# Kernel tuning notes

Hardware: AMD Instinct MI355X
Metric: run time of the kernel (lower is better)

## Reference

```python
import jax, jax.numpy as jnp
import numpy as np
from jax import lax

B, H, W, CIN = 1, 100, 100, 1024
A = 9                      # len(anc_sizes)*len(anc_ratios)
C_BOT = 512
PRE, POST, IOU_THR = 6000, 300, 0.7   # eval path (training=False)


def setup_inputs() -> dict:
    key = jax.random.key(0)
    ks = jax.random.split(key, 9)
    std = 0.01  # RandomNormal(0, 0.01) as in the keras module
    feats = jax.random.normal(ks[0], (B, H, W, CIN), jnp.float32)
    centers = jax.random.uniform(ks[1], (B, H, W, A, 2), jnp.float32)
    wh = jax.random.uniform(ks[2], (B, H, W, A, 2), jnp.float32, minval=0.05, maxval=0.3)
    ancs = jnp.concatenate([centers, wh], axis=-1)          # ccwh, normalized
    ancs_valid = jnp.ones((B, H, W, A), jnp.float32)
    W_b = jax.random.normal(ks[3], (CIN, C_BOT), jnp.float32) * std
    b_b = jnp.zeros((C_BOT,), jnp.float32)
    W_cls = jax.random.normal(ks[4], (C_BOT, A), jnp.float32) * std
    b_cls = jnp.zeros((A,), jnp.float32)
    W_reg = jax.random.normal(ks[5], (C_BOT, A * 4), jnp.float32) * std
    b_reg = jnp.zeros((A * 4,), jnp.float32)
    return dict(feats=feats, ancs=ancs, ancs_valid=ancs_valid,
                W_b=W_b, b_b=b_b, W_cls=W_cls, b_cls=b_cls, W_reg=W_reg, b_reg=b_reg)


def _pairwise_iou(boxes):
    # boxes: [N,4] xyxy
    x1, y1, x2, y2 = boxes[:, 0], boxes[:, 1], boxes[:, 2], boxes[:, 3]
    area = (x2 - x1) * (y2 - y1)                              # [N]
    ix1 = jnp.maximum(x1[:, None], x1[None, :])
    iy1 = jnp.maximum(y1[:, None], y1[None, :])
    ix2 = jnp.minimum(x2[:, None], x2[None, :])
    iy2 = jnp.minimum(y2[:, None], y2[None, :])
    inter = jnp.maximum(ix2 - ix1, 0.0) * jnp.maximum(iy2 - iy1, 0.0)
    union = area[:, None] + area[None, :] - inter
    return inter / jnp.maximum(union, 1e-9)


def _nms_keep(boxes, valid):
    # greedy NMS over score-sorted boxes -> keep mask [N]
    iou = _pairwise_iou(boxes)
    n = boxes.shape[0]

    def step(keep_mask, i):
        suppressed = jnp.any(keep_mask & (iou[i] > IOU_THR))
        k = (~suppressed) & valid[i]
        return keep_mask.at[i].set(k), None

    keep, _ = lax.scan(step, jnp.zeros((n,), bool), jnp.arange(n))
    return keep


def _extract_proposals(cls_pred, reg_pred, ancs):
    grid_w, grid_h = cls_pred.shape[1], cls_pred.shape[2]
    scores = cls_pred.reshape(-1)           # [B*H*W*A]
    offs = reg_pred.reshape(-1, 4)
    anc = ancs.reshape(-1, 4)               # ccwh
    # apply_offsets: standard RPN decode
    xy = anc[:, :2] + offs[:, :2] * anc[:, 2:]
    wh = anc[:, 2:] * jnp.exp(offs[:, 2:])
    boxes = jnp.concatenate([xy - wh / 2, xy + wh / 2], axis=-1)   # ccwh -> xyxy
    boxes = jnp.clip(boxes, 0.0, 1.0)
    sizes = (boxes[:, 2:] - boxes[:, :2]) * jnp.array([grid_w, grid_h], jnp.float32)
    ok = jnp.all(sizes >= 1.0, axis=-1)
    # masked sort replaces boolean filtering (jit-safe); sigmoid scores are > 0,
    # so -1 marks filtered-out proposals
    masked = jnp.where(ok, scores, -1.0)
    top_scores, top_idx = lax.top_k(masked, PRE)     # descending
    top_boxes = boxes[top_idx]
    valid = top_scores > -0.5
    keep = _nms_keep(lax.stop_gradient(top_boxes), valid)
    # first POST kept boxes (in score order), zero-padded to fixed shape
    n = PRE
    prio = jnp.where(keep, jnp.arange(n), n + jnp.arange(n))
    order = jnp.argsort(prio)[:POST]
    out = jnp.where(keep[order][:, None], top_boxes[order], 0.0)
    return out


def reference(feats, ancs, ancs_valid, W_b, b_b, W_cls, b_cls, W_reg, b_reg):
    h = jax.nn.relu(jnp.einsum('bhwc,cd->bhwd', feats, W_b) + b_b)   # 1x1 conv
    cls_pred = jax.nn.sigmoid(jnp.einsum('bhwd,da->bhwa', h, W_cls) + b_cls)
    reg_pred = (jnp.einsum('bhwd,dk->bhwk', h, W_reg) + b_reg).reshape(B, H, W, A, 4)
    proposals = _extract_proposals(cls_pred, reg_pred, ancs)
    return cls_pred, reg_pred, proposals
```

## Files before the change

### kernel.cpp

```cpp
#include <hip/hip_runtime.h>
#include <math.h>

typedef unsigned int U32;
typedef unsigned long long U64;

#define NBOX   90000
#define NPIX   10000
#define KDIM   1024
#define CBOT   512
#define PRE_N  6000
#define POST_N 300
#define NWORD  94
#define MROWS  6016

#define OFF_H       0ULL
#define OFF_BOXES   20480000ULL
#define OFF_KEYS    21920000ULL
#define OFF_MASKT   22280000ULL
#define OFF_SEL     26804032ULL
#define OFF_SBOX    26852032ULL
#define OFF_VALIDW  26948032ULL
#define OFF_KEEPW   26948800ULL
#define OFF_HIST    26949568ULL
#define OFF_CNT     26950592ULL
#define OFF_TIE     26950848ULL
#define WS_NEED     26967232ULL


__global__ __launch_bounds__(256, 4) void k_gemm1(
    const float* __restrict__ A, const float* __restrict__ W,
    const float* __restrict__ bias, float* __restrict__ H,
    U32* __restrict__ hist, U32* __restrict__ cnt, U32* __restrict__ validw32)
{
  int t = threadIdx.x;
  if (blockIdx.x == 0) {
    hist[t] = 0;
    if (t < 64)  cnt[t] = (t == 1) ? (U32)PRE_N : 0u;
    if (t < 188) validw32[t] = 0;
  }
  int bid = blockIdx.x;
  int c = bid & 7;
  int s = bid >> 3;
  int x = s / 10;
  int yy = c * 10 + (s % 10);
  if (yy >= 79) return;
  __shared__ float As[16][132];
  __shared__ float Bs[16][68];
  int m0 = yy * 128, n0 = x * 64;
  int tm = t >> 4, tn = t & 15;
  int ar = t >> 1, ac = (t & 1) << 3;
  int bk = t >> 4, bc = (t & 15) << 2;
  float acc[8][4];
#pragma unroll
  for (int i = 0; i < 8; ++i)
#pragma unroll
    for (int j = 0; j < 4; ++j) acc[i][j] = 0.f;

  int arow = m0 + ar;
  float4 a0 = make_float4(0.f,0.f,0.f,0.f), a1 = a0;
  if (arow < NPIX) {
    a0 = *(const float4*)&A[(size_t)arow * KDIM + ac];
    a1 = *(const float4*)&A[(size_t)arow * KDIM + ac + 4];
  }
  float4 b0 = *(const float4*)&W[(size_t)bk * CBOT + n0 + bc];

  for (int k0 = 0; k0 < KDIM; k0 += 16) {
    __syncthreads();
    As[ac+0][ar] = a0.x; As[ac+1][ar] = a0.y; As[ac+2][ar] = a0.z; As[ac+3][ar] = a0.w;
    As[ac+4][ar] = a1.x; As[ac+5][ar] = a1.y; As[ac+6][ar] = a1.z; As[ac+7][ar] = a1.w;
    *(float4*)&Bs[bk][bc] = b0;
    __syncthreads();
    if (k0 + 16 < KDIM) {
      int kn = k0 + 16;
      if (arow < NPIX) {
        a0 = *(const float4*)&A[(size_t)arow * KDIM + kn + ac];
        a1 = *(const float4*)&A[(size_t)arow * KDIM + kn + ac + 4];
      }
      b0 = *(const float4*)&W[(size_t)(kn + bk) * CBOT + n0 + bc];
    }
#pragma unroll
    for (int kk = 0; kk < 16; ++kk) {
      float4 av0 = *(float4*)&As[kk][tm*8];
      float4 av1 = *(float4*)&As[kk][tm*8+4];
      float4 bv0 = *(float4*)&Bs[kk][tn*4];
      float am[8] = {av0.x,av0.y,av0.z,av0.w,av1.x,av1.y,av1.z,av1.w};
      float bm[4] = {bv0.x,bv0.y,bv0.z,bv0.w};
#pragma unroll
      for (int i = 0; i < 8; ++i)
#pragma unroll
        for (int j = 0; j < 4; ++j)
          acc[i][j] = fmaf(am[i], bm[j], acc[i][j]);
    }
  }
  float4 bb = *(const float4*)&bias[n0 + tn*4];
  float bm[4] = {bb.x, bb.y, bb.z, bb.w};
#pragma unroll
  for (int i = 0; i < 8; ++i) {
    int r = m0 + tm*8 + i;
    if (r < NPIX) {
      float4 o;
      o.x = fmaxf(acc[i][0] + bm[0], 0.f);
      o.y = fmaxf(acc[i][1] + bm[1], 0.f);
      o.z = fmaxf(acc[i][2] + bm[2], 0.f);
      o.w = fmaxf(acc[i][3] + bm[3], 0.f);
      *(float4*)&H[(size_t)r * CBOT + n0 + tn*4] = o;
    }
  }
}

__global__ __launch_bounds__(256) void k_heads(
    const float* __restrict__ H, const float* __restrict__ Wc,
    const float* __restrict__ bc, const float* __restrict__ Wr,
    const float* __restrict__ br, float* __restrict__ outCls,
    float* __restrict__ outReg)
{
  __shared__ float hs[4][516];
  int t = threadIdx.x;
  int p0 = blockIdx.x * 4;
  for (int q = t; q < 512; q += 256) {
    int row = q >> 7, off = (q & 127) << 2;
    *(float4*)&hs[row][off] = *(const float4*)&H[(size_t)(p0 + row) * CBOT + off];
  }
  __syncthreads();
  if (t < 180) {
    int pl = t / 45, c = t % 45;
    const float* wp; int stride; float bval;
    if (c < 9) { wp = Wc + c;       stride = 9;  bval = bc[c]; }
    else       { wp = Wr + (c - 9); stride = 36; bval = br[c - 9]; }
    float s = 0.f;
    const float* hrow = hs[pl];
    for (int k = 0; k < CBOT; k += 4) {
      float4 hv = *(const float4*)&hrow[k];
      s = fmaf(hv.x, wp[(size_t)(k+0)*stride], s);
      s = fmaf(hv.y, wp[(size_t)(k+1)*stride], s);
      s = fmaf(hv.z, wp[(size_t)(k+2)*stride], s);
      s = fmaf(hv.w, wp[(size_t)(k+3)*stride], s);
    }
    s += bval;
    int p = p0 + pl;
    if (c < 9) outCls[(size_t)p*9 + c] = 1.f / (1.f + expf(-s));
    else       outReg[(size_t)p*36 + (c - 9)] = s;
  }
}

__global__ __launch_bounds__(256) void k_decode(
    const float* __restrict__ outCls, const float* __restrict__ outReg,
    const float* __restrict__ ancs, float* __restrict__ boxes,
    U32* __restrict__ keys, U32* __restrict__ hist)
{
  __shared__ U32 lh[256];
  int t = threadIdx.x;
  int tid = blockIdx.x * 256 + t;
  lh[t] = 0;
  __syncthreads();
  if (tid < NBOX) {
    float sc = outCls[tid];
    float4 of = *(const float4*)&outReg[(size_t)tid*4];
    float4 an = *(const float4*)&ancs[(size_t)tid*4];
    float cx = an.x + of.x * an.z;
    float cy = an.y + of.y * an.w;
    float ww = an.z * expf(of.z);
    float hh = an.w * expf(of.w);
    float x1 = fminf(fmaxf(cx - ww * 0.5f, 0.f), 1.f);
    float y1 = fminf(fmaxf(cy - hh * 0.5f, 0.f), 1.f);
    float x2 = fminf(fmaxf(cx + ww * 0.5f, 0.f), 1.f);
    float y2 = fminf(fmaxf(cy + hh * 0.5f, 0.f), 1.f);
    bool ok = ((x2 - x1) * 100.f >= 1.f) && ((y2 - y1) * 100.f >= 1.f);
    float msc = ok ? sc : -1.f;
    U32 u = __float_as_uint(msc);
    U32 key = (u & 0x80000000u) ? ~u : (u | 0x80000000u);
    keys[tid] = key;
    *(float4*)&boxes[(size_t)tid*4] = make_float4(x1, y1, x2, y2);
    atomicAdd(&lh[key >> 24], 1u);
  }
  __syncthreads();
  if (lh[t]) atomicAdd(&hist[t], lh[t]);
}

__global__ __launch_bounds__(256) void k_scan(
    U32* __restrict__ hist, U32* __restrict__ cnt, int level)
{
  __shared__ U32 lh[256];
  int t = threadIdx.x;
  lh[t] = hist[t];
  __syncthreads();
  if (t == 0) {
    U32 target = cnt[1];
    U32 cum = 0;
    int d = 255;
    while (d > 0) {
      U32 hh = lh[d];
      if (cum + hh >= target) break;
      cum += hh; --d;
    }
    cnt[0] |= ((U32)d) << (24 - 8*level);
    cnt[1] = target - cum;
    cnt[2] += cum;
  }
  __syncthreads();
  hist[t] = 0;
}

__global__ __launch_bounds__(256) void k_hist(
    const U32* __restrict__ keys, U32* __restrict__ hist,
    const U32* __restrict__ cnt, int level)
{
  __shared__ U32 lh[256];
  int t = threadIdx.x;
  int tid = blockIdx.x * 256 + t;
  lh[t] = 0;
  __syncthreads();
  if (tid < NBOX) {
    U32 k = keys[tid];
    U32 prefix = cnt[0];
    int shift = 32 - 8*level;
    if ((k >> shift) == (prefix >> shift)) {
      U32 bin = (k >> (24 - 8*level)) & 0xFFu;
      atomicAdd(&lh[bin], 1u);
    }
  }
  __syncthreads();
  if (lh[t]) atomicAdd(&hist[t], lh[t]);
}

__global__ __launch_bounds__(256) void k_compact(
    const U32* __restrict__ keys, U32* __restrict__ cnt,
    U64* __restrict__ sel, U32* __restrict__ tiebuf)
{
  int tid = blockIdx.x * 256 + threadIdx.x;
  if (tid >= NBOX) return;
  U32 k = keys[tid];
  U32 T = cnt[0];
  if (k > T) {
    U32 p = atomicAdd(&cnt[8], 1u);
    sel[p] = ((U64)k << 32) | (U64)(0xFFFFFFFFu - (U32)tid);
  } else if (k == T) {
    U32 p = atomicAdd(&cnt[9], 1u);
    if (p < 4096) tiebuf[p] = (U32)tid;
  }
}

__global__ __launch_bounds__(256) void k_ties(
    U32* __restrict__ cnt, const U32* __restrict__ tiebuf, U64* __restrict__ sel)
{
  __shared__ U32 tb[4096];
  int t = threadIdx.x;
  U32 m = cnt[9]; if (m > 4096u) m = 4096u;
  U32 need = cnt[1];
  U32 cgt  = cnt[2];
  U32 T    = cnt[0];
  for (U32 j = t; j < m; j += 256) tb[j] = tiebuf[j];
  __syncthreads();
  for (U32 x = t; x < m; x += 256) {
    U32 my = tb[x];
    U32 r = 0;
    for (U32 j = 0; j < m; ++j) r += (tb[j] < my) ? 1u : 0u;
    if (r < need) sel[cgt + r] = ((U64)T << 32) | (U64)(0xFFFFFFFFu - my);
  }
}

__global__ __launch_bounds__(256) void k_rank(
    const U64* __restrict__ sel, const float* __restrict__ boxes,
    float* __restrict__ sboxes, U64* __restrict__ validw)
{
  __shared__ U64 ss[PRE_N];
  int t = threadIdx.x;
  for (int j = t; j < PRE_N; j += 256) ss[j] = sel[j];
  __syncthreads();
  int i = blockIdx.x * 256 + t;
  if (i >= PRE_N) return;
  U64 C = ss[i];
  int r = 0;
  for (int j = 0; j < PRE_N; ++j) r += (ss[j] > C) ? 1 : 0;
  U32 key = (U32)(C >> 32);
  U32 idx = 0xFFFFFFFFu - (U32)(C & 0xFFFFFFFFull);
  *(float4*)&sboxes[(size_t)r*4] = *(const float4*)&boxes[(size_t)idx*4];
  if (key & 0x80000000u)
    atomicOr(&validw[r >> 6], 1ull << (r & 63));
}

__global__ __launch_bounds__(256) void k_mask(
    const float* __restrict__ sboxes, U64* __restrict__ maskT)
{
  int cw = blockIdx.x, rg = blockIdx.y;
  if (rg < cw) return;
  int t = threadIdx.x;
  int lane = t & 63, wv = t >> 6;
  int col = cw * 64 + lane;
  int cc = (col < PRE_N) ? col : (PRE_N - 1);
  float4 cb = *(const float4*)&sboxes[(size_t)cc*4];
  float areaC = (cb.z - cb.x) * (cb.w - cb.y);
  bool colok = (col < PRE_N);
  for (int rr = wv; rr < 64; rr += 4) {
    int row = rg * 64 + rr;
    U64 word = 0;
    if (row < PRE_N) {
      float4 rb = *(const float4*)&sboxes[(size_t)row*4];
      float areaR = (rb.z - rb.x) * (rb.w - rb.y);
      float ix1 = fmaxf(rb.x, cb.x), iy1 = fmaxf(rb.y, cb.y);
      float ix2 = fminf(rb.z, cb.z), iy2 = fminf(rb.w, cb.w);
      float inter = fmaxf(ix2 - ix1, 0.f) * fmaxf(iy2 - iy1, 0.f);
      float uni = areaR + areaC - inter;
      float iou = inter / fmaxf(uni, 1e-9f);
      word = __ballot(colok && (iou > 0.7f));
    }
    if (lane == 0) maskT[(size_t)cw * MROWS + row] = word;
  }
}

__global__ __launch_bounds__(512, 1) void k_nms(
    const U64* __restrict__ maskT, const U64* __restrict__ validw,
    U64* __restrict__ keepw)
{
  __shared__ U32 sup[MROWS];
  __shared__ U64 vws[NWORD];
  __shared__ U64 kwsh;
  int t = threadIdx.x;
  int wave = t >> 6, lane = t & 63;
  for (int i = t; i < MROWS; i += 512) sup[i] = 0;
  if (t < NWORD) vws[t] = validw[t];
  U64 low = (lane == 0) ? 0ull : (~0ull >> (64 - lane));
  U64 intra = (wave == 0) ? maskT[lane] : 0ull;
  __syncthreads();
  for (int c = 0; c < NWORD; ++c) {
    if (wave == 0) {
      U64 vw = vws[c];
      bool alive = (((vw >> lane) & 1ull) != 0ull) && (sup[c * 64 + lane] == 0u);
      U64 aliveW = __ballot(alive);
      bool myconf = alive && ((intra & aliveW & low) != 0ull);
      U64 confW = __ballot(myconf);
      U64 keep = aliveW & ~confW;
      U64 rem = confW;
      while (rem) {
        int b = __ffsll((unsigned long long)rem) - 1;
        rem &= rem - 1;
        U64 Z = __ballot((intra & keep & low) == 0ull);
        if ((Z >> b) & 1ull) keep |= (1ull << b);
      }
      if (lane == 0) { keepw[c] = keep; kwsh = keep; }
      if (c + 1 < NWORD)
        intra = maskT[(size_t)(c + 1) * MROWS + (c + 1) * 64 + lane];
    }
    __syncthreads();
    U64 keep = kwsh;
    if (keep) {
      const U64* colp = maskT + (size_t)c * MROWS;
      int base = (c + 1) * 64;
      U64 m[12];
#pragma unroll
      for (int q = 0; q < 12; ++q) {
        int i = base + q * 512 + t;
        int ic = (i > MROWS - 1) ? (MROWS - 1) : i;
        m[q] = colp[ic];
      }
#pragma unroll
      for (int q = 0; q < 12; ++q) {
        int i = base + q * 512 + t;
        if (i < PRE_N && (m[q] & keep)) sup[i] = 1u;
      }
    }
    __syncthreads();
  }
}

__global__ __launch_bounds__(256) void k_out(
    const U64* __restrict__ keepw, const float* __restrict__ sboxes,
    float* __restrict__ prop)
{
  __shared__ U64 kw[NWORD];
  __shared__ U32 pre[NWORD + 1];
  int t = threadIdx.x;
  if (t < NWORD) kw[t] = keepw[t];
  __syncthreads();
  if (t == 0) {
    U32 s = 0;
    for (int w = 0; w < NWORD; ++w) { pre[w] = s; s += (U32)__popcll(kw[w]); }
    pre[NWORD] = s;
  }
  for (int x = t; x < POST_N * 4; x += 256) prop[x] = 0.f;
  __syncthreads();
  for (int i = t; i < PRE_N; i += 256) {
    int w = i >> 6, b = i & 63;
    if ((kw[w] >> b) & 1ull) {
      U64 lowb = (b == 0) ? 0ull : (~0ull >> (64 - b));
      U32 r = pre[w] + (U32)__popcll(kw[w] & lowb);
      if (r < POST_N)
        *(float4*)&prop[(size_t)r*4] = *(const float4*)&sboxes[(size_t)i*4];
    }
  }
}

extern "C" void kernel_launch(void* const* d_in, const int* in_sizes, int n_in,
                              void* d_out, int out_size, void* d_ws, size_t ws_size,
                              hipStream_t stream)
{
  (void)in_sizes; (void)n_in; (void)out_size;
  if (ws_size < WS_NEED) return;

  const float* feats = (const float*)d_in[0];
  const float* ancs  = (const float*)d_in[1];
  const float* W_b   = (const float*)d_in[3];
  const float* b_b   = (const float*)d_in[4];
  const float* W_cls = (const float*)d_in[5];
  const float* b_cls = (const float*)d_in[6];
  const float* W_reg = (const float*)d_in[7];
  const float* b_reg = (const float*)d_in[8];

  float* out    = (float*)d_out;
  float* outCls = out;
  float* outReg = out + 90000;
  float* prop   = out + 450000;

  char* ws = (char*)d_ws;
  float* H      = (float*)(ws + OFF_H);
  float* boxes  = (float*)(ws + OFF_BOXES);
  U32*   keys   = (U32*)  (ws + OFF_KEYS);
  U64*   maskT  = (U64*)  (ws + OFF_MASKT);
  U64*   sel    = (U64*)  (ws + OFF_SEL);
  float* sboxes = (float*)(ws + OFF_SBOX);
  U64*   validw = (U64*)  (ws + OFF_VALIDW);
  U64*   keepw  = (U64*)  (ws + OFF_KEEPW);
  U32*   hist   = (U32*)  (ws + OFF_HIST);
  U32*   cnt    = (U32*)  (ws + OFF_CNT);
  U32*   tiebuf = (U32*)  (ws + OFF_TIE);

  k_gemm1<<<dim3(640), dim3(256), 0, stream>>>(feats, W_b, b_b, H,
                                               hist, cnt, (U32*)validw);
  k_heads<<<dim3(2500), dim3(256), 0, stream>>>(H, W_cls, b_cls, W_reg, b_reg,
                                                outCls, outReg);
  k_decode<<<dim3(352), dim3(256), 0, stream>>>(outCls, outReg, ancs,
                                                boxes, keys, hist);
  k_scan<<<dim3(1), dim3(256), 0, stream>>>(hist, cnt, 0);
  for (int lv = 1; lv <= 3; ++lv) {
    k_hist<<<dim3(352), dim3(256), 0, stream>>>(keys, hist, cnt, lv);
    k_scan<<<dim3(1), dim3(256), 0, stream>>>(hist, cnt, lv);
  }
  k_compact<<<dim3(352), dim3(256), 0, stream>>>(keys, cnt, sel, tiebuf);
  k_ties<<<dim3(1), dim3(256), 0, stream>>>(cnt, tiebuf, sel);
  k_rank<<<dim3(24), dim3(256), 0, stream>>>(sel, boxes, sboxes, validw);
  k_mask<<<dim3(94, 94), dim3(256), 0, stream>>>(sboxes, maskT);
  k_nms<<<dim3(1), dim3(512), 0, stream>>>(maskT, validw, keepw);
  k_out<<<dim3(1), dim3(256), 0, stream>>>(keepw, sboxes, prop);
}
```

Baseline: 544.0 us.

## Double-buffer GEMM shared tiles and prefetch NMS mask columns before decision

The first GEMM now uses two shared-memory buffers for the A and B tiles. The next tile's global loads and stores are issued around the current tile's FMA loop, so only one barrier is needed per k-step instead of two. In the NMS kernel, each column's mask words are loaded before wave 0 resolves the intra-word keep decision, which overlaps the global load latency with the serial ballot work. The cost is twice the GEMM shared memory, which may reduce occupancy, and mask loads that now happen even for words where nothing is kept.

```diff
diff --git a/kernel.cpp b/kernel.cpp
--- a/kernel.cpp
+++ b/kernel.cpp
@@ -44,8 +44,8 @@
   int x = s / 10;
   int yy = c * 10 + (s % 10);
   if (yy >= 79) return;
-  __shared__ float As[16][132];
-  __shared__ float Bs[16][68];
+  __shared__ float As[2][16][132];
+  __shared__ float Bs[2][16][68];
   int m0 = yy * 128, n0 = x * 64;
   int tm = t >> 4, tn = t & 15;
   int ar = t >> 1, ac = (t & 1) << 3;
@@ -57,32 +57,39 @@
     for (int j = 0; j < 4; ++j) acc[i][j] = 0.f;
 
   int arow = m0 + ar;
-  float4 a0 = make_float4(0.f,0.f,0.f,0.f), a1 = a0;
-  if (arow < NPIX) {
-    a0 = *(const float4*)&A[(size_t)arow * KDIM + ac];
-    a1 = *(const float4*)&A[(size_t)arow * KDIM + ac + 4];
-  }
-  float4 b0 = *(const float4*)&W[(size_t)bk * CBOT + n0 + bc];
-
+  {
+    float4 a0 = make_float4(0.f,0.f,0.f,0.f), a1 = a0;
+    if (arow < NPIX) {
+      a0 = *(const float4*)&A[(size_t)arow * KDIM + ac];
+      a1 = *(const float4*)&A[(size_t)arow * KDIM + ac + 4];
+    }
+    float4 b0 = *(const float4*)&W[(size_t)bk * CBOT + n0 + bc];
+    As[0][ac+0][ar] = a0.x; As[0][ac+1][ar] = a0.y;
+    As[0][ac+2][ar] = a0.z; As[0][ac+3][ar] = a0.w;
+    As[0][ac+4][ar] = a1.x; As[0][ac+5][ar] = a1.y;
+    As[0][ac+6][ar] = a1.z; As[0][ac+7][ar] = a1.w;
+    *(float4*)&Bs[0][bk][bc] = b0;
+  }
+  __syncthreads();
+
+  int cur = 0;
   for (int k0 = 0; k0 < KDIM; k0 += 16) {
-    __syncthreads();
-    As[ac+0][ar] = a0.x; As[ac+1][ar] = a0.y; As[ac+2][ar] = a0.z; As[ac+3][ar] = a0.w;
-    As[ac+4][ar] = a1.x; As[ac+5][ar] = a1.y; As[ac+6][ar] = a1.z; As[ac+7][ar] = a1.w;
-    *(float4*)&Bs[bk][bc] = b0;
-    __syncthreads();
-    if (k0 + 16 < KDIM) {
+    int nxt = cur ^ 1;
+    bool more = (k0 + 16) < KDIM;
+    float4 na0 = make_float4(0.f,0.f,0.f,0.f), na1 = na0, nb0 = na0;
+    if (more) {
       int kn = k0 + 16;
       if (arow < NPIX) {
-        a0 = *(const float4*)&A[(size_t)arow * KDIM + kn + ac];
-        a1 = *(const float4*)&A[(size_t)arow * KDIM + kn + ac + 4];
+        na0 = *(const float4*)&A[(size_t)arow * KDIM + kn + ac];
+        na1 = *(const float4*)&A[(size_t)arow * KDIM + kn + ac + 4];
       }
-      b0 = *(const float4*)&W[(size_t)(kn + bk) * CBOT + n0 + bc];
+      nb0 = *(const float4*)&W[(size_t)(kn + bk) * CBOT + n0 + bc];
     }
 #pragma unroll
     for (int kk = 0; kk < 16; ++kk) {
-      float4 av0 = *(float4*)&As[kk][tm*8];
-      float4 av1 = *(float4*)&As[kk][tm*8+4];
-      float4 bv0 = *(float4*)&Bs[kk][tn*4];
+      float4 av0 = *(float4*)&As[cur][kk][tm*8];
+      float4 av1 = *(float4*)&As[cur][kk][tm*8+4];
+      float4 bv0 = *(float4*)&Bs[cur][kk][tn*4];
       float am[8] = {av0.x,av0.y,av0.z,av0.w,av1.x,av1.y,av1.z,av1.w};
       float bm[4] = {bv0.x,bv0.y,bv0.z,bv0.w};
 #pragma unroll
@@ -91,6 +98,15 @@
         for (int j = 0; j < 4; ++j)
           acc[i][j] = fmaf(am[i], bm[j], acc[i][j]);
     }
+    if (more) {
+      As[nxt][ac+0][ar] = na0.x; As[nxt][ac+1][ar] = na0.y;
+      As[nxt][ac+2][ar] = na0.z; As[nxt][ac+3][ar] = na0.w;
+      As[nxt][ac+4][ar] = na1.x; As[nxt][ac+5][ar] = na1.y;
+      As[nxt][ac+6][ar] = na1.z; As[nxt][ac+7][ar] = na1.w;
+      *(float4*)&Bs[nxt][bk][bc] = nb0;
+    }
+    __syncthreads();
+    cur = nxt;
   }
   float4 bb = *(const float4*)&bias[n0 + tn*4];
   float bm[4] = {bb.x, bb.y, bb.z, bb.w};
@@ -323,6 +339,15 @@
   U64 intra = (wave == 0) ? maskT[lane] : 0ull;
   __syncthreads();
   for (int c = 0; c < NWORD; ++c) {
+    const U64* colp = maskT + (size_t)c * MROWS;
+    int base = (c + 1) * 64;
+    U64 m[12];
+#pragma unroll
+    for (int q = 0; q < 12; ++q) {
+      int i = base + q * 512 + t;
+      int ic = (i > MROWS - 1) ? (MROWS - 1) : i;
+      m[q] = colp[ic];
+    }
     if (wave == 0) {
       U64 vw = vws[c];
       bool alive = (((vw >> lane) & 1ull) != 0ull) && (sup[c * 64 + lane] == 0u);
@@ -343,21 +368,10 @@
     }
     __syncthreads();
     U64 keep = kwsh;
-    if (keep) {
-      const U64* colp = maskT + (size_t)c * MROWS;
-      int base = (c + 1) * 64;
-      U64 m[12];
-#pragma unroll
-      for (int q = 0; q < 12; ++q) {
-        int i = base + q * 512 + t;
-        int ic = (i > MROWS - 1) ? (MROWS - 1) : i;
-        m[q] = colp[ic];
-      }
-#pragma unroll
-      for (int q = 0; q < 12; ++q) {
-        int i = base + q * 512 + t;
-        if (i < PRE_N && (m[q] & keep)) sup[i] = 1u;
-      }
+#pragma unroll
+    for (int q = 0; q < 12; ++q) {
+      int i = base + q * 512 + t;
+      if (i < PRE_N && (m[q] & keep)) sup[i] = 1u;
     }
     __syncthreads();
   }
```

Result: slower. 2.036 ms (+274.3%).
